# Performance work log

Measured on AMD Instinct MI355X. Metric: run time of the kernel, lower is better.

The kernel has to match this reference:

```python
import jax, jax.numpy as jnp
import numpy as np

N_NODES = 100000   # destination-node segments for edge_softmax
N_GRAPHS = 128     # batched graphs for sum_edges readout
E = 1_600_000      # total edges (avg degree 16)
F = 64             # in_feats
NEG_SLOPE = 0.01   # torch LeakyReLU default


def setup_inputs() -> dict:
    key = jax.random.key(0)
    k1, k2, k3, k4 = jax.random.split(key, 4)
    edge_feats = jax.random.normal(k1, (E, F), jnp.float32)
    W = jax.random.normal(k2, (F, 1), jnp.float32) / np.sqrt(F)
    b = jnp.zeros((1,), jnp.float32)
    edge_dst = jnp.sort(jax.random.randint(k3, (E,), 0, N_NODES)).astype(jnp.int32)
    graph_ids = jnp.sort(jax.random.randint(k4, (E,), 0, N_GRAPHS)).astype(jnp.int32)
    return {"edge_feats": edge_feats, "W": W, "b": b,
            "edge_dst": edge_dst, "graph_ids": graph_ids}


def reference(edge_feats, W, b, edge_dst, graph_ids):
    # per-edge scalar score: Linear(F,1) + LeakyReLU
    s = jax.nn.leaky_relu(edge_feats @ W + b, negative_slope=NEG_SLOPE)[:, 0]  # [E]
    # edge_softmax: numerically-stable softmax over edges sharing a dst node
    m = jax.ops.segment_max(s, edge_dst, num_segments=N_NODES, indices_are_sorted=True)   # [N]
    ex = jnp.exp(s - m[edge_dst])                                                          # [E]
    den = jax.ops.segment_sum(ex, edge_dst, num_segments=N_NODES, indices_are_sorted=True) # [N]
    weights = (ex / den[edge_dst])[:, None]                                                # [E,1]
    # dgl.sum_edges(g, 'e', 'w'): per-graph weighted sum of edge features
    h_g_sum = jax.ops.segment_sum(edge_feats * weights, graph_ids,
                                  num_segments=N_GRAPHS, indices_are_sorted=True)          # [G,F]
    return h_g_sum, weights
```

## Files before the change

### kernel.cpp

```cpp
#include <hip/hip_runtime.h>
#include <math.h>

#define E_TOTAL 1600000
#define NN 100000
#define NG 128
#define FF 64
#define NGROUPS (E_TOTAL / 64)

__global__ __launch_bounds__(256) void init_kernel(float* den, float* hg) {
    int i = blockIdx.x * blockDim.x + threadIdx.x;
    if (i < NN) den[i] = 0.0f;
    if (i < NG * FF) hg[i] = 0.0f;
}

__global__ __launch_bounds__(256) void score_kernel(
        const float4* __restrict__ feats4, const float4* __restrict__ W4,
        const float* __restrict__ b, const int* __restrict__ dst,
        float* __restrict__ exbuf, float* __restrict__ den) {
    int tid  = blockIdx.x * blockDim.x + threadIdx.x;
    int lane = threadIdx.x & 63;
    int wave = tid >> 6;
    int nw   = (gridDim.x * blockDim.x) >> 6;
    int sub  = lane >> 4;
    int sl   = lane & 15;
    float4 w = W4[sl];
    float bias = b[0];
    for (int ebase = wave * 4; ebase < E_TOTAL; ebase += nw * 4) {
        int e = ebase + sub;
        float4 v = feats4[(size_t)e * 16 + sl];
        float dq = v.x * w.x + v.y * w.y + v.z * w.z + v.w * w.w;
        dq += __shfl_xor(dq, 1);
        dq += __shfl_xor(dq, 2);
        dq += __shfl_xor(dq, 4);
        dq += __shfl_xor(dq, 8);
        float ex = 0.0f; int d = -1;
        if (sl == 0) {
            float sv = dq + bias;
            sv = sv > 0.0f ? sv : 0.01f * sv;
            ex = __expf(sv);
            exbuf[e] = ex;
            d = dst[e];
        }
        float sp = __shfl_up(ex, 16); int dp = __shfl_up(d, 16);
        if (sub >= 1 && dp == d) ex += sp;
        sp = __shfl_up(ex, 32); dp = __shfl_up(d, 32);
        if (sub >= 2 && dp == d) ex += sp;
        int dn = __shfl_down(d, 16);
        if (sl == 0 && (sub == 3 || dn != d)) atomicAdd(&den[d], ex);
    }
}

__device__ __forceinline__ void flush_acc(float4& acc, int cur_g, int lane,
                                          float* __restrict__ hg) {
    acc.x += __shfl_xor(acc.x, 16); acc.y += __shfl_xor(acc.y, 16);
    acc.z += __shfl_xor(acc.z, 16); acc.w += __shfl_xor(acc.w, 16);
    acc.x += __shfl_xor(acc.x, 32); acc.y += __shfl_xor(acc.y, 32);
    acc.z += __shfl_xor(acc.z, 32); acc.w += __shfl_xor(acc.w, 32);
    if (lane < 16) {
        float* p = hg + cur_g * 64 + lane * 4;
        atomicAdd(p + 0, acc.x); atomicAdd(p + 1, acc.y);
        atomicAdd(p + 2, acc.z); atomicAdd(p + 3, acc.w);
    }
    acc.x = acc.y = acc.z = acc.w = 0.0f;
}

__global__ __launch_bounds__(256) void wsum_kernel(
        const float4* __restrict__ feats4, const float* __restrict__ exbuf,
        const float* __restrict__ den, const int* __restrict__ dst,
        const int* __restrict__ gid, float* __restrict__ wout,
        float* __restrict__ hg) {
    int tid  = blockIdx.x * blockDim.x + threadIdx.x;
    int lane = threadIdx.x & 63;
    int wave = tid >> 6;
    int nwaves = (gridDim.x * blockDim.x) >> 6;
    int gpw = (NGROUPS + nwaves - 1) / nwaves;
    int g0 = wave * gpw;
    if (g0 >= NGROUPS) return;
    int g1 = min(g0 + gpw, NGROUPS);
    int q = lane >> 4;
    float4 acc = {0.f, 0.f, 0.f, 0.f};
    int cur_g = -1;
    for (int grp = g0; grp < g1; ++grp) {
        int e = grp * 64 + lane;
        float w = exbuf[e] / den[dst[e]];
        wout[e] = w;
        int gg = gid[e];
        int gfirst = __builtin_amdgcn_readfirstlane(gg);
        bool uni = (__ballot(gg != gfirst) == 0ULL);
        const float4* frow = feats4 + (size_t)grp * 64 * 16;
        if (uni) {
            if (gfirst != cur_g) {
                if (cur_g >= 0) flush_acc(acc, cur_g, lane, hg);
                cur_g = gfirst;
            }
            #pragma unroll 4
            for (int it = 0; it < 16; ++it) {
                float we = __shfl(w, it * 4 + q);
                float4 v = frow[it * 64 + lane];
                acc.x += v.x * we; acc.y += v.y * we;
                acc.z += v.z * we; acc.w += v.w * we;
            }
        } else {
            int sl = lane & 15;
            for (int j = 0; j < 64; ++j) {
                int gj = __shfl(gg, j);
                if (gj != cur_g) {
                    if (cur_g >= 0) flush_acc(acc, cur_g, lane, hg);
                    cur_g = gj;
                }
                if (q == (j & 3)) {
                    float we = __shfl(w, j);
                    float4 v = frow[j * 16 + sl];
                    acc.x += v.x * we; acc.y += v.y * we;
                    acc.z += v.z * we; acc.w += v.w * we;
                }
            }
        }
    }
    if (cur_g >= 0) flush_acc(acc, cur_g, lane, hg);
}

extern "C" void kernel_launch(void* const* d_in, const int* in_sizes, int n_in,
                              void* d_out, int out_size, void* d_ws, size_t ws_size,
                              hipStream_t stream) {
    const float* feats = (const float*)d_in[0];
    const float* W     = (const float*)d_in[1];
    const float* b     = (const float*)d_in[2];
    const int*   dst   = (const int*)d_in[3];
    const int*   gid   = (const int*)d_in[4];

    float* out   = (float*)d_out;
    float* hg    = out;
    float* wout  = out + NG * FF;

    float* exbuf = (float*)d_ws;
    float* den   = exbuf + E_TOTAL;

    init_kernel<<<(NN + 255) / 256, 256, 0, stream>>>(den, hg);
    score_kernel<<<2048, 256, 0, stream>>>((const float4*)feats, (const float4*)W,
                                           b, dst, exbuf, den);
    wsum_kernel<<<1024, 256, 0, stream>>>((const float4*)feats, exbuf, den,
                                          dst, gid, wout, hg);
}
```

Measured before the change: 636.3 us.

## Read edge features once via per-node unnormalized sums, normalize per node

Drops the max subtraction and builds an unnormalized weighted feature sum per destination node (T) and the denominator in a single pass over the edge features. Per-graph sums then come from scaling T by 1/den in a small node-level pass, with a straddle fix-up for nodes whose edges cross a graph boundary. This removes the second full read of the 400MB feature matrix. In exchange it adds a 25.6MB T buffer with zeroing and atomics, skips max-subtraction (risk of overflow for large scores), and caps straddle records at MAXSTRAD.

```diff
diff --git a/kernel.cpp b/kernel.cpp
--- a/kernel.cpp
+++ b/kernel.cpp
@@ -5,119 +5,224 @@
 #define NN 100000
 #define NG 128
 #define FF 64
-#define NGROUPS (E_TOTAL / 64)
-
-__global__ __launch_bounds__(256) void init_kernel(float* den, float* hg) {
+#define NCHUNK (E_TOTAL / 4)
+#define MAXSTRAD 2048
+
+__global__ __launch_bounds__(256) void init_kernel(
+        float* __restrict__ T, float* __restrict__ den,
+        int* __restrict__ nodeg, float* __restrict__ hg,
+        int* __restrict__ scount) {
     int i = blockIdx.x * blockDim.x + threadIdx.x;
-    if (i < NN) den[i] = 0.0f;
+    if (i < NN * 64) T[i] = 0.0f;
+    if (i < NN) { den[i] = 0.0f; nodeg[i] = 0; }
     if (i < NG * FF) hg[i] = 0.0f;
-}
-
-__global__ __launch_bounds__(256) void score_kernel(
+    if (i == 0) *scount = 0;
+}
+
+__device__ __forceinline__ void seg_flush(float4& acc, float& dacc,
+        int cur_d, int cur_g, int lane,
+        float* __restrict__ T, float* __restrict__ den,
+        int* __restrict__ nodeg) {
+    float ax = acc.x, ay = acc.y, az = acc.z, aw = acc.w, dd = dacc;
+    ax += __shfl_xor(ax, 16); ay += __shfl_xor(ay, 16);
+    az += __shfl_xor(az, 16); aw += __shfl_xor(aw, 16);
+    dd += __shfl_xor(dd, 16);
+    ax += __shfl_xor(ax, 32); ay += __shfl_xor(ay, 32);
+    az += __shfl_xor(az, 32); aw += __shfl_xor(aw, 32);
+    dd += __shfl_xor(dd, 32);
+    if (lane < 16) {
+        float* p = T + (size_t)cur_d * 64 + lane * 4;
+        atomicAdd(p + 0, ax); atomicAdd(p + 1, ay);
+        atomicAdd(p + 2, az); atomicAdd(p + 3, aw);
+    } else if (lane == 16) {
+        atomicAdd(&den[cur_d], dd);
+    } else if (lane == 17) {
+        atomicMax(&nodeg[cur_d], cur_g);
+    }
+    acc.x = acc.y = acc.z = acc.w = 0.0f;
+    dacc = 0.0f;
+}
+
+__global__ __launch_bounds__(256) void pass1_kernel(
         const float4* __restrict__ feats4, const float4* __restrict__ W4,
         const float* __restrict__ b, const int* __restrict__ dst,
-        float* __restrict__ exbuf, float* __restrict__ den) {
+        const int* __restrict__ gid,
+        float* __restrict__ exbuf, float* __restrict__ den,
+        float* __restrict__ T, int* __restrict__ nodeg,
+        int* __restrict__ scount, int* __restrict__ slist) {
     int tid  = blockIdx.x * blockDim.x + threadIdx.x;
     int lane = threadIdx.x & 63;
     int wave = tid >> 6;
     int nw   = (gridDim.x * blockDim.x) >> 6;
-    int sub  = lane >> 4;
-    int sl   = lane & 15;
+    int cpw  = (NCHUNK + nw - 1) / nw;
+    int c0 = wave * cpw;
+    if (c0 >= NCHUNK) return;
+    int c1 = min(c0 + cpw, NCHUNK);
+    int q = lane >> 4, sl = lane & 15;
     float4 w = W4[sl];
     float bias = b[0];
-    for (int ebase = wave * 4; ebase < E_TOTAL; ebase += nw * 4) {
-        int e = ebase + sub;
-        float4 v = feats4[(size_t)e * 16 + sl];
-        float dq = v.x * w.x + v.y * w.y + v.z * w.z + v.w * w.w;
-        dq += __shfl_xor(dq, 1);
-        dq += __shfl_xor(dq, 2);
-        dq += __shfl_xor(dq, 4);
-        dq += __shfl_xor(dq, 8);
-        float ex = 0.0f; int d = -1;
-        if (sl == 0) {
-            float sv = dq + bias;
-            sv = sv > 0.0f ? sv : 0.01f * sv;
-            ex = __expf(sv);
-            exbuf[e] = ex;
-            d = dst[e];
-        }
-        float sp = __shfl_up(ex, 16); int dp = __shfl_up(d, 16);
-        if (sub >= 1 && dp == d) ex += sp;
-        sp = __shfl_up(ex, 32); dp = __shfl_up(d, 32);
-        if (sub >= 2 && dp == d) ex += sp;
-        int dn = __shfl_down(d, 16);
-        if (sl == 0 && (sub == 3 || dn != d)) atomicAdd(&den[d], ex);
-    }
-}
-
-__device__ __forceinline__ void flush_acc(float4& acc, int cur_g, int lane,
-                                          float* __restrict__ hg) {
-    acc.x += __shfl_xor(acc.x, 16); acc.y += __shfl_xor(acc.y, 16);
-    acc.z += __shfl_xor(acc.z, 16); acc.w += __shfl_xor(acc.w, 16);
-    acc.x += __shfl_xor(acc.x, 32); acc.y += __shfl_xor(acc.y, 32);
-    acc.z += __shfl_xor(acc.z, 32); acc.w += __shfl_xor(acc.w, 32);
-    if (lane < 16) {
-        float* p = hg + cur_g * 64 + lane * 4;
-        atomicAdd(p + 0, acc.x); atomicAdd(p + 1, acc.y);
-        atomicAdd(p + 2, acc.z); atomicAdd(p + 3, acc.w);
-    }
-    acc.x = acc.y = acc.z = acc.w = 0.0f;
-}
-
-__global__ __launch_bounds__(256) void wsum_kernel(
-        const float4* __restrict__ feats4, const float* __restrict__ exbuf,
-        const float* __restrict__ den, const int* __restrict__ dst,
-        const int* __restrict__ gid, float* __restrict__ wout,
-        float* __restrict__ hg) {
+
+    int cur_d, cur_g;
+    if (c0 == 0) { cur_d = -1; cur_g = -1; }
+    else { cur_d = dst[c0 * 4 - 1]; cur_g = gid[c0 * 4 - 1]; }
+    float4 acc = {0.f, 0.f, 0.f, 0.f};
+    float dacc = 0.0f;
+
+    float4 v = feats4[(size_t)c0 * 64 + lane];
+    int d = dst[c0 * 4 + q];
+    int g = gid[c0 * 4 + q];
+
+    for (int c = c0; c < c1; ++c) {
+        float4 cv = v; int cd = d, cg = g;
+        if (c + 1 < c1) {
+            v = feats4[(size_t)(c + 1) * 64 + lane];
+            d = dst[(c + 1) * 4 + q];
+            g = gid[(c + 1) * 4 + q];
+        }
+        float dq = cv.x * w.x + cv.y * w.y + cv.z * w.z + cv.w * w.w;
+        dq += __shfl_xor(dq, 1); dq += __shfl_xor(dq, 2);
+        dq += __shfl_xor(dq, 4); dq += __shfl_xor(dq, 8);
+        float s = dq + bias;
+        s = s > 0.0f ? s : 0.01f * s;
+        float ex = __expf(s);
+        if (sl == 0) exbuf[c * 4 + q] = ex;
+
+        int d0 = __builtin_amdgcn_readfirstlane(cd);
+        int g0 = __builtin_amdgcn_readfirstlane(cg);
+        if (__ballot(cd != d0 || cg != g0) == 0ULL) {
+            if (d0 != cur_d) {
+                if (cur_d >= 0) seg_flush(acc, dacc, cur_d, cur_g, lane, T, den, nodeg);
+                cur_d = d0; cur_g = g0;
+            } else if (g0 != cur_g) {
+                if (lane == 0) {
+                    int idx = atomicAdd(scount, 1);
+                    if (idx < MAXSTRAD) slist[idx] = c * 4;
+                }
+                cur_g = g0;
+            }
+            acc.x += cv.x * ex; acc.y += cv.y * ex;
+            acc.z += cv.z * ex; acc.w += cv.w * ex;
+            dacc += (sl == 0) ? ex : 0.0f;
+        } else {
+            #pragma unroll
+            for (int qq = 0; qq < 4; ++qq) {
+                int dqq = __shfl(cd, qq * 16);
+                int gqq = __shfl(cg, qq * 16);
+                if (dqq != cur_d) {
+                    if (cur_d >= 0) seg_flush(acc, dacc, cur_d, cur_g, lane, T, den, nodeg);
+                    cur_d = dqq; cur_g = gqq;
+                } else if (gqq != cur_g) {
+                    if (lane == 0) {
+                        int idx = atomicAdd(scount, 1);
+                        if (idx < MAXSTRAD) slist[idx] = c * 4 + qq;
+                    }
+                    cur_g = gqq;
+                }
+                float m = (q == qq) ? ex : 0.0f;
+                acc.x += cv.x * m; acc.y += cv.y * m;
+                acc.z += cv.z * m; acc.w += cv.w * m;
+                dacc += (sl == 0) ? m : 0.0f;
+            }
+        }
+    }
+    if (cur_d >= 0) seg_flush(acc, dacc, cur_d, cur_g, lane, T, den, nodeg);
+}
+
+__global__ __launch_bounds__(256) void pass2a_kernel(
+        const float4* __restrict__ T4, const float* __restrict__ den,
+        const int* __restrict__ nodeg, float* __restrict__ hg) {
+    const int NCH = NN / 4;
     int tid  = blockIdx.x * blockDim.x + threadIdx.x;
     int lane = threadIdx.x & 63;
     int wave = tid >> 6;
-    int nwaves = (gridDim.x * blockDim.x) >> 6;
-    int gpw = (NGROUPS + nwaves - 1) / nwaves;
-    int g0 = wave * gpw;
-    if (g0 >= NGROUPS) return;
-    int g1 = min(g0 + gpw, NGROUPS);
+    int nw   = (gridDim.x * blockDim.x) >> 6;
+    int cpw  = (NCH + nw - 1) / nw;
+    int c0 = wave * cpw;
+    if (c0 >= NCH) return;
+    int c1 = min(c0 + cpw, NCH);
     int q = lane >> 4;
-    float4 acc = {0.f, 0.f, 0.f, 0.f};
+    double ax = 0, ay = 0, az = 0, aw = 0;
     int cur_g = -1;
-    for (int grp = g0; grp < g1; ++grp) {
-        int e = grp * 64 + lane;
-        float w = exbuf[e] / den[dst[e]];
-        wout[e] = w;
-        int gg = gid[e];
-        int gfirst = __builtin_amdgcn_readfirstlane(gg);
-        bool uni = (__ballot(gg != gfirst) == 0ULL);
-        const float4* frow = feats4 + (size_t)grp * 64 * 16;
-        if (uni) {
-            if (gfirst != cur_g) {
-                if (cur_g >= 0) flush_acc(acc, cur_g, lane, hg);
-                cur_g = gfirst;
+
+    for (int c = c0; c < c1; ++c) {
+        int node = c * 4 + q;
+        float4 tv = T4[(size_t)c * 64 + lane];
+        float dn = den[node];
+        int g = nodeg[node];
+        float inv = dn > 0.0f ? 1.0f / dn : 0.0f;
+        int g0 = __builtin_amdgcn_readfirstlane(g);
+        bool uni = (__ballot(g != g0) == 0ULL);
+        if (uni && g0 == cur_g) {
+            ax += (double)(tv.x * inv); ay += (double)(tv.y * inv);
+            az += (double)(tv.z * inv); aw += (double)(tv.w * inv);
+        } else {
+            #pragma unroll
+            for (int qq = 0; qq < 4; ++qq) {
+                int gqq = __shfl(g, qq * 16);
+                if (gqq != cur_g) {
+                    if (cur_g >= 0) {
+                        double bx = ax, by = ay, bz = az, bw = aw;
+                        bx += __shfl_xor(bx, 16); by += __shfl_xor(by, 16);
+                        bz += __shfl_xor(bz, 16); bw += __shfl_xor(bw, 16);
+                        bx += __shfl_xor(bx, 32); by += __shfl_xor(by, 32);
+                        bz += __shfl_xor(bz, 32); bw += __shfl_xor(bw, 32);
+                        if (lane < 16) {
+                            float* p = hg + cur_g * 64 + lane * 4;
+                            atomicAdd(p + 0, (float)bx); atomicAdd(p + 1, (float)by);
+                            atomicAdd(p + 2, (float)bz); atomicAdd(p + 3, (float)bw);
+                        }
+                        ax = ay = az = aw = 0;
+                    }
+                    cur_g = gqq;
+                }
+                float m = (q == qq) ? inv : 0.0f;
+                ax += (double)(tv.x * m); ay += (double)(tv.y * m);
+                az += (double)(tv.z * m); aw += (double)(tv.w * m);
             }
-            #pragma unroll 4
-            for (int it = 0; it < 16; ++it) {
-                float we = __shfl(w, it * 4 + q);
-                float4 v = frow[it * 64 + lane];
-                acc.x += v.x * we; acc.y += v.y * we;
-                acc.z += v.z * we; acc.w += v.w * we;
-            }
-        } else {
-            int sl = lane & 15;
-            for (int j = 0; j < 64; ++j) {
-                int gj = __shfl(gg, j);
-                if (gj != cur_g) {
-                    if (cur_g >= 0) flush_acc(acc, cur_g, lane, hg);
-                    cur_g = gj;
-                }
-                if (q == (j & 3)) {
-                    float we = __shfl(w, j);
-                    float4 v = frow[j * 16 + sl];
-                    acc.x += v.x * we; acc.y += v.y * we;
-                    acc.z += v.z * we; acc.w += v.w * we;
-                }
-            }
-        }
-    }
-    if (cur_g >= 0) flush_acc(acc, cur_g, lane, hg);
+        }
+    }
+    if (cur_g >= 0) {
+        ax += __shfl_xor(ax, 16); ay += __shfl_xor(ay, 16);
+        az += __shfl_xor(az, 16); aw += __shfl_xor(aw, 16);
+        ax += __shfl_xor(ax, 32); ay += __shfl_xor(ay, 32);
+        az += __shfl_xor(az, 32); aw += __shfl_xor(aw, 32);
+        if (lane < 16) {
+            float* p = hg + cur_g * 64 + lane * 4;
+            atomicAdd(p + 0, (float)ax); atomicAdd(p + 1, (float)ay);
+            atomicAdd(p + 2, (float)az); atomicAdd(p + 3, (float)aw);
+        }
+    }
+}
+
+__global__ __launch_bounds__(256) void pass2b_kernel(
+        const float* __restrict__ feats, const float* __restrict__ exbuf,
+        const float* __restrict__ den, const int* __restrict__ dst,
+        const int* __restrict__ gid, const int* __restrict__ scount,
+        const int* __restrict__ slist, float* __restrict__ hg) {
+    int nrec = *scount; if (nrec > MAXSTRAD) nrec = MAXSTRAD;
+    int lane = threadIdx.x & 63;
+    int wave = (blockIdx.x * blockDim.x + threadIdx.x) >> 6;
+    int nw   = (gridDim.x * blockDim.x) >> 6;
+    for (int r = wave; r < nrec; r += nw) {
+        int e  = slist[r];
+        int d_ = dst[e];
+        int g1 = gid[e], g0 = gid[e - 1];
+        int lo = e - 1;
+        while (lo > 0 && dst[lo - 1] == d_) --lo;
+        float invd = 1.0f / den[d_];
+        float acc = 0.0f;
+        for (int ee = lo; ee < e; ++ee)
+            acc += feats[(size_t)ee * 64 + lane] * (exbuf[ee] * invd);
+        atomicAdd(&hg[g0 * 64 + lane],  acc);
+        atomicAdd(&hg[g1 * 64 + lane], -acc);
+    }
+}
+
+__global__ __launch_bounds__(256) void weights_kernel(
+        const float* __restrict__ exbuf, const float* __restrict__ den,
+        const int* __restrict__ dst, float* __restrict__ wout) {
+    int i = blockIdx.x * blockDim.x + threadIdx.x;
+    if (i < E_TOTAL) wout[i] = exbuf[i] / den[dst[i]];
 }
 
 extern "C" void kernel_launch(void* const* d_in, const int* in_sizes, int n_in,
@@ -129,16 +234,23 @@
     const int*   dst   = (const int*)d_in[3];
     const int*   gid   = (const int*)d_in[4];
 
-    float* out   = (float*)d_out;
-    float* hg    = out;
-    float* wout  = out + NG * FF;
-
-    float* exbuf = (float*)d_ws;
+    float* out  = (float*)d_out;
+    float* hg   = out;
+    float* wout = out + NG * FF;
+
+    float* T     = (float*)d_ws;
+    float* exbuf = T + (size_t)NN * 64;
     float* den   = exbuf + E_TOTAL;
-
-    init_kernel<<<(NN + 255) / 256, 256, 0, stream>>>(den, hg);
-    score_kernel<<<2048, 256, 0, stream>>>((const float4*)feats, (const float4*)W,
-                                           b, dst, exbuf, den);
-    wsum_kernel<<<1024, 256, 0, stream>>>((const float4*)feats, exbuf, den,
-                                          dst, gid, wout, hg);
-}
+    int*   nodeg = (int*)(den + NN);
+    int*   scount = nodeg + NN;
+    int*   slist  = scount + 1;
+
+    init_kernel<<<(NN * 64 + 255) / 256, 256, 0, stream>>>(T, den, nodeg, hg, scount);
+    pass1_kernel<<<2048, 256, 0, stream>>>((const float4*)feats, (const float4*)W,
+                                           b, dst, gid, exbuf, den, T, nodeg,
+                                           scount, slist);
+    pass2a_kernel<<<512, 256, 0, stream>>>((const float4*)T, den, nodeg, hg);
+    pass2b_kernel<<<4, 256, 0, stream>>>(feats, exbuf, den, dst, gid,
+                                         scount, slist, hg);
+    weights_kernel<<<(E_TOTAL + 255) / 256, 256, 0, stream>>>(exbuf, den, dst, wout);
+}
```

Result: slower. 659.9 us (+3.7%).
